# Kernel optimization log

Measured on AMD Instinct MI355X. Metric: run time of the kernel, lower is better.

The kernel has to match this reference:

```python
import jax, jax.numpy as jnp
import numpy as np

N, F = 100000, 64   # input (up) nodes, feature dim
M, K = 100000, 32   # down nodes, neighbors per node


def setup_inputs() -> dict:
    key = jax.random.key(0)
    k1, k2, k3, k4 = jax.random.split(key, 4)
    features = jax.random.normal(k1, (N, F), dtype=jnp.float32)
    sel_idx_up = jax.random.randint(k2, (N, 1), 0, M, dtype=jnp.int64)
    weights_down = jax.random.uniform(k3, (M, K, 1), dtype=jnp.float32)
    nidx_down = jax.random.randint(k4, (M, K), 0, M, dtype=jnp.int64)
    return {
        "features": features,
        "weights_down": weights_down,
        "sel_idx_up": sel_idx_up,
        "nidx_down": nidx_down,
    }


def reference(features, weights_down, sel_idx_up, nidx_down):
    # PullDown, mode='mean', weights=None.
    m = weights_down.shape[0]
    f_dim = features.shape[1]
    # tf.scatter_nd: duplicate indices accumulate (add)
    down_f = jnp.zeros((m, f_dim), dtype=features.dtype).at[sel_idx_up[:, 0]].add(features)
    # acc_knn weighted mean over K neighbors; nidx == -1 means invalid (zero contribution)
    mask = nidx_down >= 0                              # [M, K]
    idx = jnp.where(mask, nidx_down, 0)
    gathered = down_f[idx] * weights_down              # [M, K, F]
    gathered = jnp.where(mask[..., None], gathered, jnp.zeros((), dtype=features.dtype))
    out = jnp.mean(gathered, axis=1)                   # divide by K, as acc_sum's *K implies
    return out.reshape(-1, f_dim)
```

## Files before the change

kernel.cpp:

```cpp
#include <hip/hip_runtime.h>
#include <hip/hip_bf16.h>

#define F_DIM 64
#define K_NB  32
#define CAP   16

typedef float        f32x4 __attribute__((ext_vector_type(4)));
typedef int          i32x4 __attribute__((ext_vector_type(4)));
typedef unsigned int u32;

__device__ inline u32 f2b(float f) {
    u32 u = __float_as_uint(f);
    u32 r = ((u >> 16) & 1u) + 0x7fffu;
    return (u + r) >> 16;
}
__device__ inline float blo(u32 u) { return __uint_as_float(u << 16); }
__device__ inline float bhi(u32 u) { return __uint_as_float(u & 0xffff0000u); }

__global__ __launch_bounds__(256) void bucket_fill_kernel(
    const int* __restrict__ sel_idx,
    int*       __restrict__ cnt,
    int*       __restrict__ bucket,
    int N)
{
    int i = blockIdx.x * blockDim.x + threadIdx.x;
    if (i >= N) return;
    int m = sel_idx[i];
    int slot = atomicAdd(&cnt[m], 1);
    if (slot < CAP) bucket[m * CAP + slot] = i;
}

__global__ __launch_bounds__(256) void build_down_f_bf16_kernel(
    const f32x4* __restrict__ features4,
    const int*   __restrict__ cnt,
    const i32x4* __restrict__ bucket4,
    unsigned short* __restrict__ down_h,
    int M)
{
    int t = blockIdx.x * blockDim.x + threadIdx.x;
    int m = t >> 4;
    int q = t & 15;
    if (m >= M) return;
    int c = cnt[m]; c = c < CAP ? c : CAP;
    i32x4 b4 = bucket4[(size_t)m * (CAP / 4)];

    int i0 = (0 < c) ? b4.x : 0;  float g0 = (0 < c) ? 1.f : 0.f;
    int i1 = (1 < c) ? b4.y : 0;  float g1 = (1 < c) ? 1.f : 0.f;
    int i2 = (2 < c) ? b4.z : 0;  float g2 = (2 < c) ? 1.f : 0.f;
    int i3 = (3 < c) ? b4.w : 0;  float g3 = (3 < c) ? 1.f : 0.f;

    f32x4 v0 = __builtin_nontemporal_load(&features4[(size_t)i0 * 16 + q]);
    f32x4 v1 = __builtin_nontemporal_load(&features4[(size_t)i1 * 16 + q]);
    f32x4 v2 = __builtin_nontemporal_load(&features4[(size_t)i2 * 16 + q]);
    f32x4 v3 = __builtin_nontemporal_load(&features4[(size_t)i3 * 16 + q]);

    f32x4 acc;
    acc.x = g0 * v0.x + g1 * v1.x + g2 * v2.x + g3 * v3.x;
    acc.y = g0 * v0.y + g1 * v1.y + g2 * v2.y + g3 * v3.y;
    acc.z = g0 * v0.z + g1 * v1.z + g2 * v2.z + g3 * v3.z;
    acc.w = g0 * v0.w + g1 * v1.w + g2 * v2.w + g3 * v3.w;

    if (c > 4) {
        const int* bk = (const int*)(bucket4 + (size_t)m * (CAP / 4));
        for (int j = 4; j < c; ++j) {
            int i = bk[j];
            f32x4 v = __builtin_nontemporal_load(&features4[(size_t)i * 16 + q]);
            acc.x += v.x; acc.y += v.y; acc.z += v.z; acc.w += v.w;
        }
    }
    uint2 o;
    o.x = f2b(acc.x) | (f2b(acc.y) << 16);
    o.y = f2b(acc.z) | (f2b(acc.w) << 16);
    *(uint2*)(down_h + (size_t)m * F_DIM + q * 4) = o;
}

__global__ __launch_bounds__(256) void gather_mean_bf16_kernel(
    const unsigned short* __restrict__ down_h,
    const f32x4*          __restrict__ weights4,
    const i32x4*          __restrict__ nidx4,
    f32x4*                __restrict__ out4,
    int M)
{
    int t = blockIdx.x * blockDim.x + threadIdx.x;
    int m = t >> 3;
    int q = t & 7;
    if (m >= M) return;

    const i32x4* ni = nidx4    + (size_t)m * (K_NB / 4);
    const f32x4* wp = weights4 + (size_t)m * (K_NB / 4);
    const unsigned char* bp = (const unsigned char*)down_h + (unsigned)q * 16u;

    float a0 = 0.f, a1 = 0.f, a2 = 0.f, a3 = 0.f;
    float a4 = 0.f, a5 = 0.f, a6 = 0.f, a7 = 0.f;

#define LOADIW(s, b) \
    i32x4 Ix##s = __builtin_nontemporal_load(ni + 2 * (b));     \
    i32x4 Iy##s = __builtin_nontemporal_load(ni + 2 * (b) + 1); \
    f32x4 Wx##s = __builtin_nontemporal_load(wp + 2 * (b));     \
    f32x4 Wy##s = __builtin_nontemporal_load(wp + 2 * (b) + 1); \
    unsigned j0##s = Ix##s.x < 0 ? 0u : (unsigned)Ix##s.x;  float w0##s = Ix##s.x < 0 ? 0.f : Wx##s.x; \
    unsigned j1##s = Ix##s.y < 0 ? 0u : (unsigned)Ix##s.y;  float w1##s = Ix##s.y < 0 ? 0.f : Wx##s.y; \
    unsigned j2##s = Ix##s.z < 0 ? 0u : (unsigned)Ix##s.z;  float w2##s = Ix##s.z < 0 ? 0.f : Wx##s.z; \
    unsigned j3##s = Ix##s.w < 0 ? 0u : (unsigned)Ix##s.w;  float w3##s = Ix##s.w < 0 ? 0.f : Wx##s.w; \
    unsigned j4##s = Iy##s.x < 0 ? 0u : (unsigned)Iy##s.x;  float w4##s = Iy##s.x < 0 ? 0.f : Wy##s.x; \
    unsigned j5##s = Iy##s.y < 0 ? 0u : (unsigned)Iy##s.y;  float w5##s = Iy##s.y < 0 ? 0.f : Wy##s.y; \
    unsigned j6##s = Iy##s.z < 0 ? 0u : (unsigned)Iy##s.z;  float w6##s = Iy##s.z < 0 ? 0.f : Wy##s.z; \
    unsigned j7##s = Iy##s.w < 0 ? 0u : (unsigned)Iy##s.w;  float w7##s = Iy##s.w < 0 ? 0.f : Wy##s.w;

#define ISSUE(s) \
    uint4 g0##s = *(const uint4*)(bp + (size_t)(j0##s * 128u)); \
    uint4 g1##s = *(const uint4*)(bp + (size_t)(j1##s * 128u)); \
    uint4 g2##s = *(const uint4*)(bp + (size_t)(j2##s * 128u)); \
    uint4 g3##s = *(const uint4*)(bp + (size_t)(j3##s * 128u)); \
    uint4 g4##s = *(const uint4*)(bp + (size_t)(j4##s * 128u)); \
    uint4 g5##s = *(const uint4*)(bp + (size_t)(j5##s * 128u)); \
    uint4 g6##s = *(const uint4*)(bp + (size_t)(j6##s * 128u)); \
    uint4 g7##s = *(const uint4*)(bp + (size_t)(j7##s * 128u));

#define ACC1(gv, wv) \
    a0 += wv * blo(gv.x); a1 += wv * bhi(gv.x); \
    a2 += wv * blo(gv.y); a3 += wv * bhi(gv.y); \
    a4 += wv * blo(gv.z); a5 += wv * bhi(gv.z); \
    a6 += wv * blo(gv.w); a7 += wv * bhi(gv.w);

#define ACCB(s) \
    ACC1(g0##s, w0##s) ACC1(g1##s, w1##s) ACC1(g2##s, w2##s) ACC1(g3##s, w3##s) \
    ACC1(g4##s, w4##s) ACC1(g5##s, w5##s) ACC1(g6##s, w6##s) ACC1(g7##s, w7##s)

    LOADIW(A, 0) ISSUE(A)
    LOADIW(B, 1) ISSUE(B)
    ACCB(A)
    __builtin_amdgcn_sched_barrier(0);
    LOADIW(C, 2) ISSUE(C)
    ACCB(B)
    __builtin_amdgcn_sched_barrier(0);
    LOADIW(D, 3) ISSUE(D)
    ACCB(C)
    __builtin_amdgcn_sched_barrier(0);
    ACCB(D)

#undef LOADIW
#undef ISSUE
#undef ACC1
#undef ACCB

    const float s = 1.0f / (float)K_NB;
    size_t o = (size_t)m * 16 + q * 2;
    f32x4 r0; r0.x = a0 * s; r0.y = a1 * s; r0.z = a2 * s; r0.w = a3 * s;
    f32x4 r1; r1.x = a4 * s; r1.y = a5 * s; r1.z = a6 * s; r1.w = a7 * s;
    __builtin_nontemporal_store(r0, &out4[o + 0]);
    __builtin_nontemporal_store(r1, &out4[o + 1]);
}

__global__ __launch_bounds__(256) void scatter_add_kernel(
    const float* __restrict__ features, const int* __restrict__ sel_idx,
    float* __restrict__ down_f, int N)
{
    int t = blockIdx.x * blockDim.x + threadIdx.x;
    int i  = t >> 5;
    int fp = (t & 31);
    if (i >= N) return;
    int dst = sel_idx[i];
    float2 v = ((const float2*)features)[(size_t)i * (F_DIM / 2) + fp];
    float* d = down_f + (size_t)dst * F_DIM + fp * 2;
    atomicAdd(d + 0, v.x);
    atomicAdd(d + 1, v.y);
}

__global__ __launch_bounds__(256) void gather_mean_f32_kernel(
    const float2* __restrict__ down_f2, const float* __restrict__ weights,
    const int* __restrict__ nidx, float2* __restrict__ out2, int M)
{
    int t  = blockIdx.x * blockDim.x + threadIdx.x;
    int m  = t >> 5;
    int fp = t & 31;
    if (m >= M) return;
    const i32x4* ni4 = (const i32x4*)(nidx    + (size_t)m * K_NB);
    const f32x4* wp4 = (const f32x4*)(weights + (size_t)m * K_NB);
    float accx = 0.f, accy = 0.f;
    #pragma unroll
    for (int q = 0; q < K_NB / 4; ++q) {
        i32x4 iv = ni4[q];
        f32x4 wv = wp4[q];
        int i0 = iv.x < 0 ? 0 : iv.x;  float w0 = iv.x < 0 ? 0.f : wv.x;
        int i1 = iv.y < 0 ? 0 : iv.y;  float w1 = iv.y < 0 ? 0.f : wv.y;
        int i2 = iv.z < 0 ? 0 : iv.z;  float w2 = iv.z < 0 ? 0.f : wv.z;
        int i3 = iv.w < 0 ? 0 : iv.w;  float w3 = iv.w < 0 ? 0.f : wv.w;
        float2 v0 = down_f2[(size_t)i0 * (F_DIM / 2) + fp];
        float2 v1 = down_f2[(size_t)i1 * (F_DIM / 2) + fp];
        float2 v2 = down_f2[(size_t)i2 * (F_DIM / 2) + fp];
        float2 v3 = down_f2[(size_t)i3 * (F_DIM / 2) + fp];
        accx += w0 * v0.x; accy += w0 * v0.y;
        accx += w1 * v1.x; accy += w1 * v1.y;
        accx += w2 * v2.x; accy += w2 * v2.y;
        accx += w3 * v3.x; accy += w3 * v3.y;
    }
    float2 r;
    r.x = accx * (1.0f / (float)K_NB);
    r.y = accy * (1.0f / (float)K_NB);
    out2[(size_t)m * (F_DIM / 2) + fp] = r;
}

extern "C" void kernel_launch(void* const* d_in, const int* in_sizes, int n_in,
                              void* d_out, int out_size, void* d_ws, size_t ws_size,
                              hipStream_t stream) {
    const float* features = (const float*)d_in[0];
    const float* weights  = (const float*)d_in[1];
    const int*   sel_idx  = (const int*)  d_in[2];
    const int*   nidx     = (const int*)  d_in[3];
    float*       out      = (float*)d_out;

    const int N = in_sizes[2];
    const int M = in_sizes[3] / K_NB;

    size_t downh_bytes  = (size_t)M * F_DIM * sizeof(unsigned short);
    size_t cnt_bytes    = (size_t)M * sizeof(int);
    size_t bucket_bytes = (size_t)M * CAP * sizeof(int);

    if (ws_size >= downh_bytes + cnt_bytes + bucket_bytes) {
        unsigned short* down_h = (unsigned short*)d_ws;
        int* cnt    = (int*)((char*)d_ws + downh_bytes);
        int* bucket = cnt + M;

        hipMemsetAsync(cnt, 0, cnt_bytes, stream);
        bucket_fill_kernel<<<(N + 255) / 256, 256, 0, stream>>>(
            sel_idx, cnt, bucket, N);
        build_down_f_bf16_kernel<<<(M * 16 + 255) / 256, 256, 0, stream>>>(
            (const f32x4*)features, cnt, (const i32x4*)bucket, down_h, M);
        gather_mean_bf16_kernel<<<(M * 8 + 255) / 256, 256, 0, stream>>>(
            down_h, (const f32x4*)weights, (const i32x4*)nidx,
            (f32x4*)out, M);
    } else {
        float* down_f = (float*)d_ws;
        hipMemsetAsync(down_f, 0, (size_t)M * F_DIM * sizeof(float), stream);
        scatter_add_kernel<<<(N * 32 + 255) / 256, 256, 0, stream>>>(
            features, sel_idx, down_f, N);
        gather_mean_f32_kernel<<<(M * 32 + 255) / 256, 256, 0, stream>>>(
            (const float2*)down_f, weights, nidx, (float2*)out, M);
    }
}
```

Measured before the change: 161.4 us.

## Compact nonzero down nodes into dense table with remap indirection

Adds a ticket kernel that assigns each down node with at least one contributor a compact slot (slot 0 is a shared zero row). The build kernel skips empty nodes and writes only compacted rows, and the gather kernel looks up the remap before fetching rows. This shrinks the bf16 gather table (about 63% of nodes are nonempty for random indices), improving cache hit rates and cutting write traffic. In exchange it adds a kernel launch, an atomic per nonempty node, and a dependent remap load before each gather load, lengthening the latency chain.

```diff
diff --git a/kernel.cpp b/kernel.cpp
--- a/kernel.cpp
+++ b/kernel.cpp
@@ -30,10 +30,29 @@
     if (slot < CAP) bucket[m * CAP + slot] = i;
 }
 
+__global__ __launch_bounds__(256) void compact_ticket_kernel(
+    const int* __restrict__ cnt,
+    int*       __restrict__ nz,
+    int*       __restrict__ remap,
+    unsigned short* __restrict__ down_h,
+    int M)
+{
+    int m = blockIdx.x * blockDim.x + threadIdx.x;
+    if (blockIdx.x == 0 && threadIdx.x < 16) {
+        uint2 z; z.x = 0u; z.y = 0u;
+        ((uint2*)down_h)[threadIdx.x] = z;
+    }
+    if (m >= M) return;
+    int slot = 0;
+    if (cnt[m] > 0) slot = 1 + atomicAdd(nz, 1);
+    remap[m] = slot;
+}
+
 __global__ __launch_bounds__(256) void build_down_f_bf16_kernel(
     const f32x4* __restrict__ features4,
     const int*   __restrict__ cnt,
     const i32x4* __restrict__ bucket4,
+    const int*   __restrict__ remap,
     unsigned short* __restrict__ down_h,
     int M)
 {
@@ -41,10 +60,13 @@
     int m = t >> 4;
     int q = t & 15;
     if (m >= M) return;
-    int c = cnt[m]; c = c < CAP ? c : CAP;
+    int c = cnt[m];
+    if (c == 0) return;
+    c = c < CAP ? c : CAP;
+    int s = remap[m];
     i32x4 b4 = bucket4[(size_t)m * (CAP / 4)];
 
-    int i0 = (0 < c) ? b4.x : 0;  float g0 = (0 < c) ? 1.f : 0.f;
+    int i0 = b4.x;
     int i1 = (1 < c) ? b4.y : 0;  float g1 = (1 < c) ? 1.f : 0.f;
     int i2 = (2 < c) ? b4.z : 0;  float g2 = (2 < c) ? 1.f : 0.f;
     int i3 = (3 < c) ? b4.w : 0;  float g3 = (3 < c) ? 1.f : 0.f;
@@ -55,10 +77,10 @@
     f32x4 v3 = __builtin_nontemporal_load(&features4[(size_t)i3 * 16 + q]);
 
     f32x4 acc;
-    acc.x = g0 * v0.x + g1 * v1.x + g2 * v2.x + g3 * v3.x;
-    acc.y = g0 * v0.y + g1 * v1.y + g2 * v2.y + g3 * v3.y;
-    acc.z = g0 * v0.z + g1 * v1.z + g2 * v2.z + g3 * v3.z;
-    acc.w = g0 * v0.w + g1 * v1.w + g2 * v2.w + g3 * v3.w;
+    acc.x = v0.x + g1 * v1.x + g2 * v2.x + g3 * v3.x;
+    acc.y = v0.y + g1 * v1.y + g2 * v2.y + g3 * v3.y;
+    acc.z = v0.z + g1 * v1.z + g2 * v2.z + g3 * v3.z;
+    acc.w = v0.w + g1 * v1.w + g2 * v2.w + g3 * v3.w;
 
     if (c > 4) {
         const int* bk = (const int*)(bucket4 + (size_t)m * (CAP / 4));
@@ -71,13 +93,14 @@
     uint2 o;
     o.x = f2b(acc.x) | (f2b(acc.y) << 16);
     o.y = f2b(acc.z) | (f2b(acc.w) << 16);
-    *(uint2*)(down_h + (size_t)m * F_DIM + q * 4) = o;
+    *(uint2*)(down_h + (size_t)s * F_DIM + q * 4) = o;
 }
 
 __global__ __launch_bounds__(256) void gather_mean_bf16_kernel(
     const unsigned short* __restrict__ down_h,
     const f32x4*          __restrict__ weights4,
     const i32x4*          __restrict__ nidx4,
+    const int*            __restrict__ remap,
     f32x4*                __restrict__ out4,
     int M)
 {
@@ -93,29 +116,49 @@
     float a0 = 0.f, a1 = 0.f, a2 = 0.f, a3 = 0.f;
     float a4 = 0.f, a5 = 0.f, a6 = 0.f, a7 = 0.f;
 
-#define LOADIW(s, b) \
+#define LOADI(s, b) \
     i32x4 Ix##s = __builtin_nontemporal_load(ni + 2 * (b));     \
     i32x4 Iy##s = __builtin_nontemporal_load(ni + 2 * (b) + 1); \
+    unsigned j0##s = Ix##s.x < 0 ? 0u : (unsigned)Ix##s.x; \
+    unsigned j1##s = Ix##s.y < 0 ? 0u : (unsigned)Ix##s.y; \
+    unsigned j2##s = Ix##s.z < 0 ? 0u : (unsigned)Ix##s.z; \
+    unsigned j3##s = Ix##s.w < 0 ? 0u : (unsigned)Ix##s.w; \
+    unsigned j4##s = Iy##s.x < 0 ? 0u : (unsigned)Iy##s.x; \
+    unsigned j5##s = Iy##s.y < 0 ? 0u : (unsigned)Iy##s.y; \
+    unsigned j6##s = Iy##s.z < 0 ? 0u : (unsigned)Iy##s.z; \
+    unsigned j7##s = Iy##s.w < 0 ? 0u : (unsigned)Iy##s.w;
+
+#define REMAP(s) \
+    unsigned r0##s = (unsigned)remap[j0##s]; \
+    unsigned r1##s = (unsigned)remap[j1##s]; \
+    unsigned r2##s = (unsigned)remap[j2##s]; \
+    unsigned r3##s = (unsigned)remap[j3##s]; \
+    unsigned r4##s = (unsigned)remap[j4##s]; \
+    unsigned r5##s = (unsigned)remap[j5##s]; \
+    unsigned r6##s = (unsigned)remap[j6##s]; \
+    unsigned r7##s = (unsigned)remap[j7##s];
+
+#define LOADW(s, b) \
     f32x4 Wx##s = __builtin_nontemporal_load(wp + 2 * (b));     \
     f32x4 Wy##s = __builtin_nontemporal_load(wp + 2 * (b) + 1); \
-    unsigned j0##s = Ix##s.x < 0 ? 0u : (unsigned)Ix##s.x;  float w0##s = Ix##s.x < 0 ? 0.f : Wx##s.x; \
-    unsigned j1##s = Ix##s.y < 0 ? 0u : (unsigned)Ix##s.y;  float w1##s = Ix##s.y < 0 ? 0.f : Wx##s.y; \
-    unsigned j2##s = Ix##s.z < 0 ? 0u : (unsigned)Ix##s.z;  float w2##s = Ix##s.z < 0 ? 0.f : Wx##s.z; \
-    unsigned j3##s = Ix##s.w < 0 ? 0u : (unsigned)Ix##s.w;  float w3##s = Ix##s.w < 0 ? 0.f : Wx##s.w; \
-    unsigned j4##s = Iy##s.x < 0 ? 0u : (unsigned)Iy##s.x;  float w4##s = Iy##s.x < 0 ? 0.f : Wy##s.x; \
-    unsigned j5##s = Iy##s.y < 0 ? 0u : (unsigned)Iy##s.y;  float w5##s = Iy##s.y < 0 ? 0.f : Wy##s.y; \
-    unsigned j6##s = Iy##s.z < 0 ? 0u : (unsigned)Iy##s.z;  float w6##s = Iy##s.z < 0 ? 0.f : Wy##s.z; \
-    unsigned j7##s = Iy##s.w < 0 ? 0u : (unsigned)Iy##s.w;  float w7##s = Iy##s.w < 0 ? 0.f : Wy##s.w;
+    float w0##s = Ix##s.x < 0 ? 0.f : Wx##s.x; \
+    float w1##s = Ix##s.y < 0 ? 0.f : Wx##s.y; \
+    float w2##s = Ix##s.z < 0 ? 0.f : Wx##s.z; \
+    float w3##s = Ix##s.w < 0 ? 0.f : Wx##s.w; \
+    float w4##s = Iy##s.x < 0 ? 0.f : Wy##s.x; \
+    float w5##s = Iy##s.y < 0 ? 0.f : Wy##s.y; \
+    float w6##s = Iy##s.z < 0 ? 0.f : Wy##s.z; \
+    float w7##s = Iy##s.w < 0 ? 0.f : Wy##s.w;
 
 #define ISSUE(s) \
-    uint4 g0##s = *(const uint4*)(bp + (size_t)(j0##s * 128u)); \
-    uint4 g1##s = *(const uint4*)(bp + (size_t)(j1##s * 128u)); \
-    uint4 g2##s = *(const uint4*)(bp + (size_t)(j2##s * 128u)); \
-    uint4 g3##s = *(const uint4*)(bp + (size_t)(j3##s * 128u)); \
-    uint4 g4##s = *(const uint4*)(bp + (size_t)(j4##s * 128u)); \
-    uint4 g5##s = *(const uint4*)(bp + (size_t)(j5##s * 128u)); \
-    uint4 g6##s = *(const uint4*)(bp + (size_t)(j6##s * 128u)); \
-    uint4 g7##s = *(const uint4*)(bp + (size_t)(j7##s * 128u));
+    uint4 g0##s = *(const uint4*)(bp + (size_t)(r0##s * 128u)); \
+    uint4 g1##s = *(const uint4*)(bp + (size_t)(r1##s * 128u)); \
+    uint4 g2##s = *(const uint4*)(bp + (size_t)(r2##s * 128u)); \
+    uint4 g3##s = *(const uint4*)(bp + (size_t)(r3##s * 128u)); \
+    uint4 g4##s = *(const uint4*)(bp + (size_t)(r4##s * 128u)); \
+    uint4 g5##s = *(const uint4*)(bp + (size_t)(r5##s * 128u)); \
+    uint4 g6##s = *(const uint4*)(bp + (size_t)(r6##s * 128u)); \
+    uint4 g7##s = *(const uint4*)(bp + (size_t)(r7##s * 128u));
 
 #define ACC1(gv, wv) \
     a0 += wv * blo(gv.x); a1 += wv * bhi(gv.x); \
@@ -127,19 +170,15 @@
     ACC1(g0##s, w0##s) ACC1(g1##s, w1##s) ACC1(g2##s, w2##s) ACC1(g3##s, w3##s) \
     ACC1(g4##s, w4##s) ACC1(g5##s, w5##s) ACC1(g6##s, w6##s) ACC1(g7##s, w7##s)
 
-    LOADIW(A, 0) ISSUE(A)
-    LOADIW(B, 1) ISSUE(B)
-    ACCB(A)
-    __builtin_amdgcn_sched_barrier(0);
-    LOADIW(C, 2) ISSUE(C)
-    ACCB(B)
-    __builtin_amdgcn_sched_barrier(0);
-    LOADIW(D, 3) ISSUE(D)
-    ACCB(C)
-    __builtin_amdgcn_sched_barrier(0);
-    ACCB(D)
-
-#undef LOADIW
+    LOADI(A, 0) REMAP(A)
+    LOADI(B, 1) REMAP(B)  LOADW(A, 0) ISSUE(A) ACCB(A)
+    LOADI(C, 2) REMAP(C)  LOADW(B, 1) ISSUE(B) ACCB(B)
+    LOADI(D, 3) REMAP(D)  LOADW(C, 2) ISSUE(C) ACCB(C)
+                          LOADW(D, 3) ISSUE(D) ACCB(D)
+
+#undef LOADI
+#undef REMAP
+#undef LOADW
 #undef ISSUE
 #undef ACC1
 #undef ACCB
@@ -213,22 +252,27 @@
     const int N = in_sizes[2];
     const int M = in_sizes[3] / K_NB;
 
-    size_t downh_bytes  = (size_t)M * F_DIM * sizeof(unsigned short);
-    size_t cnt_bytes    = (size_t)M * sizeof(int);
+    size_t downh_bytes  = (size_t)(M + 1) * F_DIM * sizeof(unsigned short);
     size_t bucket_bytes = (size_t)M * CAP * sizeof(int);
-
-    if (ws_size >= downh_bytes + cnt_bytes + bucket_bytes) {
+    size_t cntnz_bytes  = (size_t)(M + 1) * sizeof(int);
+    size_t remap_bytes  = (size_t)M * sizeof(int);
+
+    if (ws_size >= downh_bytes + bucket_bytes + cntnz_bytes + remap_bytes) {
         unsigned short* down_h = (unsigned short*)d_ws;
-        int* cnt    = (int*)((char*)d_ws + downh_bytes);
-        int* bucket = cnt + M;
-
-        hipMemsetAsync(cnt, 0, cnt_bytes, stream);
+        int* bucket = (int*)((char*)d_ws + downh_bytes);
+        int* cnt    = (int*)((char*)d_ws + downh_bytes + bucket_bytes);
+        int* nz     = cnt + M;
+        int* remap  = nz + 1;
+
+        hipMemsetAsync(cnt, 0, cntnz_bytes, stream);
         bucket_fill_kernel<<<(N + 255) / 256, 256, 0, stream>>>(
             sel_idx, cnt, bucket, N);
+        compact_ticket_kernel<<<(M + 255) / 256, 256, 0, stream>>>(
+            cnt, nz, remap, down_h, M);
         build_down_f_bf16_kernel<<<(M * 16 + 255) / 256, 256, 0, stream>>>(
-            (const f32x4*)features, cnt, (const i32x4*)bucket, down_h, M);
+            (const f32x4*)features, cnt, (const i32x4*)bucket, remap, down_h, M);
         gather_mean_bf16_kernel<<<(M * 8 + 255) / 256, 256, 0, stream>>>(
-            down_h, (const f32x4*)weights, (const i32x4*)nidx,
+            down_h, (const f32x4*)weights, (const i32x4*)nidx, remap,
             (f32x4*)out, M);
     } else {
         float* down_f = (float*)d_ws;
```

After: 191.0 us. +18.3%, slower.
